# Optimization experiments

Hardware: AMD Instinct MI355X
Metric: run time of the kernel (lower is better)

## Reference

```python
import jax, jax.numpy as jnp
import numpy as np

N, E, IN_DIM, HID, OUT = 50000, 800000, 128, 128, 64


def setup_inputs() -> dict:
    key = jax.random.key(0)
    k = jax.random.split(key, 6)
    h = jax.random.normal(k[0], (N, IN_DIM), dtype=jnp.float32)
    edge_index = jax.random.randint(k[1], (2, E), 0, N, dtype=jnp.int64)
    s_in, s_hid = 1.0 / np.sqrt(IN_DIM), 1.0 / np.sqrt(HID)
    W_gcn = jax.random.uniform(k[2], (IN_DIM, HID), jnp.float32, -s_in, s_in)
    b_gcn = jnp.zeros((HID,), jnp.float32)
    W_fc = jax.random.uniform(k[3], (HID, OUT), jnp.float32, -s_hid, s_hid)
    b_fc = jax.random.uniform(k[4], (OUT,), jnp.float32, -s_hid, s_hid)
    return {"h": h, "edge_index": edge_index, "W_gcn": W_gcn,
            "b_gcn": b_gcn, "W_fc": W_fc, "b_fc": b_fc}


def reference(h, edge_index, W_gcn, b_gcn, W_fc, b_fc):
    n = h.shape[0]
    # GCNConv: transform, add self-loops, symmetric normalization, scatter-add
    x = h @ W_gcn                                   # [N, HID]
    loop = jnp.arange(n, dtype=edge_index.dtype)
    row = jnp.concatenate([edge_index[0], loop])    # source nodes
    col = jnp.concatenate([edge_index[1], loop])    # destination nodes
    deg = jax.ops.segment_sum(jnp.ones_like(col, dtype=x.dtype), col,
                              num_segments=n)       # in-degree incl. self-loop
    dinv = jnp.where(deg > 0, jax.lax.rsqrt(deg), 0.0)
    norm = dinv[row] * dinv[col]                    # [E+N]
    msg = x[row] * norm[:, None]                    # gather + scale
    agg = jax.ops.segment_sum(msg, col, num_segments=n) + b_gcn
    # ReLU then projection
    return jax.nn.relu(agg) @ W_fc + b_fc
```

## Files before the change

kernel.cpp:

```cpp
#include <hip/hip_runtime.h>

#define N_NODES 50000
#define N_EDGES 800000
#define NBKT 782
#define BINB 196
#define CASTB 391
#define SLOTC 20
#define SBKT (BINB * SLOTC)
#define BCAP 1792
#define ESTRIDE 1792
#define SECAP 1792
#define UTS 136

typedef __attribute__((ext_vector_type(4))) float floatx4;
typedef __attribute__((ext_vector_type(8))) _Float16 half8;
typedef __attribute__((ext_vector_type(4))) _Float16 half4;
typedef __attribute__((ext_vector_type(2))) _Float16 half2v;

#define O_C     0UL
#define O_DEG   613120UL
#define O_PTR   813184UL
#define O_W1    1013248UL
#define O_W2    1046016UL
#define O_ESRC  1062400UL
#define O_STG   3865216UL
#define O_H16   16126976UL

__global__ __launch_bounds__(256) void k_bin(const int* __restrict__ ei,
                                             const float* __restrict__ h,
                                             int* __restrict__ C,
                                             unsigned* __restrict__ staging,
                                             const float* __restrict__ Wg,
                                             const float* __restrict__ Wf,
                                             _Float16* __restrict__ W1,
                                             _Float16* __restrict__ W2,
                                             _Float16* __restrict__ h16) {
    int b = blockIdx.x, t = threadIdx.x;
    if (b >= BINB + 96) {
        int wb = b - (BINB + 96);
        int nb = wb * 128;
        int nn = min(128, N_NODES - nb);
        if (nn <= 0) return;
        const floatx4* src = (const floatx4*)(h + (size_t)nb * 128);
        half4* dst = (half4*)(h16 + (size_t)nb * 128);
        int nq = nn * 32;
        for (int i = t; i < nq; i += 256) {
            floatx4 v = src[i];
            half4 o;
            o[0] = (_Float16)v[0]; o[1] = (_Float16)v[1];
            o[2] = (_Float16)v[2]; o[3] = (_Float16)v[3];
            dst[i] = o;
        }
        return;
    }
    if (b >= BINB) {
        int wb = b - BINB;
        if (wb < 64) {
            int i = wb * 256 + t;
            int n = i >> 7, k = i & 127;
            W1[i] = (_Float16)Wg[k * 128 + n];
        } else {
            int i = (wb - 64) * 256 + t;
            int n = i >> 7, k = i & 127;
            W2[i] = (_Float16)Wf[k * 64 + n];
        }
        return;
    }
    __shared__ int cnt[NBKT];
    __shared__ int s_i64;
    if (t < 64) {
        unsigned w = ((const unsigned*)ei)[2 * t + 1];
        unsigned long long m = __ballot(w == 0u);
        if (t == 0) s_i64 = (__popcll(m) >= 60) ? 1 : 0;
    }
    for (int i = t; i < NBKT; i += 256) cnt[i] = 0;
    __syncthreads();
    bool i64 = s_i64 != 0;
    int e0 = b * 4096 + t * 16;
    int sv[16], dvv[16];
    if (i64) {
        const int4* ps = (const int4*)(ei) + (e0 >> 1);
        const int4* pd = (const int4*)(ei + 2 * (size_t)N_EDGES) + (e0 >> 1);
#pragma unroll
        for (int g = 0; g < 8; ++g) {
            if (e0 + 2 * g < N_EDGES) {
                int4 s4 = ps[g], d4 = pd[g];
                sv[2 * g] = s4.x; sv[2 * g + 1] = s4.z;
                dvv[2 * g] = d4.x; dvv[2 * g + 1] = d4.z;
            } else { dvv[2 * g] = -1; dvv[2 * g + 1] = -1; }
        }
    } else {
        const int4* ps = (const int4*)(ei) + (e0 >> 2);
        const int4* pd = (const int4*)(ei + (size_t)N_EDGES) + (e0 >> 2);
#pragma unroll
        for (int g = 0; g < 4; ++g) {
            if (e0 + 4 * g < N_EDGES) {
                int4 s4 = ps[g], d4 = pd[g];
                sv[4 * g] = s4.x; sv[4 * g + 1] = s4.y; sv[4 * g + 2] = s4.z; sv[4 * g + 3] = s4.w;
                dvv[4 * g] = d4.x; dvv[4 * g + 1] = d4.y; dvv[4 * g + 2] = d4.z; dvv[4 * g + 3] = d4.w;
            } else { dvv[4 * g] = -1; dvv[4 * g + 1] = -1; dvv[4 * g + 2] = -1; dvv[4 * g + 3] = -1; }
        }
    }
    unsigned pk[16]; int rk[16]; short bk[16];
#pragma unroll
    for (int j = 0; j < 16; ++j) {
        int d = dvv[j];
        if (d >= 0 && e0 + j < N_EDGES) {
            int bkt = d >> 6;
            bk[j] = (short)bkt;
            pk[j] = (unsigned)sv[j] | ((unsigned)(d & 63) << 16);
            rk[j] = atomicAdd(&cnt[bkt], 1);
        } else bk[j] = -1;
    }
    __syncthreads();
    for (int i = t; i < NBKT; i += 256)
        C[(size_t)b * NBKT + i] = cnt[i];
#pragma unroll
    for (int j = 0; j < 16; ++j) {
        if (bk[j] >= 0 && rk[j] < SLOTC)
            staging[(size_t)bk[j] * SBKT + b * SLOTC + rk[j]] = pk[j];
    }
}

__global__ __launch_bounds__(256) void k_sort(const unsigned* __restrict__ staging,
                                              const int* __restrict__ C,
                                              int* __restrict__ ptr,
                                              int* __restrict__ deg_g,
                                              unsigned short* __restrict__ esrc) {
    __shared__ unsigned se[BCAP];
    __shared__ int lcnt[64];
    __shared__ int cur[64];
    __shared__ int rbase[BINB];
    __shared__ int rcnt[BINB];
    __shared__ int wsum[4];
    __shared__ int s_tot;
    int b = blockIdx.x, t = threadIdx.x;
    int nbase = b * 64;
    int nn = min(64, N_NODES - nbase);
    if (nn <= 0) return;
    int lane = t & 63, wid = t >> 6;
    if (t < 64) lcnt[t] = 0;
    int c = (t < BINB) ? min(C[(size_t)t * NBKT + b], SLOTC) : 0;
    int x = c;
#pragma unroll
    for (int off = 1; off < 64; off <<= 1) {
        int y = __shfl_up(x, off);
        if (lane >= off) x += y;
    }
    if (lane == 63) wsum[wid] = x;
    __syncthreads();
    int wpre = 0;
#pragma unroll
    for (int w = 0; w < 4; ++w) if (w < wid) wpre += wsum[w];
    int excl = wpre + x - c;
    if (t < BINB) { rbase[t] = excl; rcnt[t] = c; }
    if (t == BINB - 1) s_tot = excl + c;
    __syncthreads();
    if (t < BINB && c > 0) {
        const unsigned* sp = staging + (size_t)b * SBKT + t * SLOTC;
        int rb = rbase[t];
        for (int k = 0; k < c; ++k) {
            unsigned p = sp[k];
            if (rb + k < BCAP) {
                se[rb + k] = p;
                atomicAdd(&lcnt[p >> 16], 1);
            }
        }
    }
    __syncthreads();
    if (t < 64) {
        int v = lcnt[t];
        int xx = v;
#pragma unroll
        for (int off = 1; off < 64; off <<= 1) {
            int y = __shfl_up(xx, off);
            if (t >= off) xx += y;
        }
        int seg = xx - v;
        if (t < nn) {
            ptr[nbase + t] = b * ESTRIDE + seg;
            deg_g[nbase + t] = v;
        }
        cur[t] = seg;
    }
    __syncthreads();
    int tot = min(s_tot, BCAP);
    unsigned short* eb = esrc + (size_t)b * ESTRIDE;
    for (int i = t; i < tot; i += 256) {
        unsigned p = se[i];
        int pos = atomicAdd(&cur[p >> 16], 1);
        if (pos < ESTRIDE) eb[pos] = (unsigned short)(p & 0xffffu);
    }
}

__global__ __launch_bounds__(256, 8) void k_aggF(const _Float16* __restrict__ h16,
                                                 const int* __restrict__ ptr,
                                                 const int* __restrict__ deg_g,
                                                 const unsigned short* __restrict__ esrc,
                                                 const _Float16* __restrict__ W1,
                                                 const _Float16* __restrict__ W2,
                                                 const float* __restrict__ bg,
                                                 const float* __restrict__ bfc,
                                                 float* __restrict__ out) {
    __shared__ _Float16 ut[16 * UTS];
    __shared__ _Float16 z[16 * UTS];
    __shared__ unsigned se32[SECAP];
    __shared__ int p16[17];
    __shared__ int deg16[16];
    __shared__ float sdv16[16];
    int t = threadIdx.x;
    int wave = t >> 6;
    int lane = t & 63;
    int nb = blockIdx.x * 16;
    if (t < 16) {
        int dg = deg_g[nb + t];
        deg16[t] = dg;
        sdv16[t] = rsqrtf((float)(dg + 1));
        p16[t] = ptr[nb + t];
    }
    __syncthreads();
    if (t == 0) p16[16] = p16[15] + deg16[15];
    __syncthreads();
    int base0 = p16[0];
    int total = p16[16] - base0;
    if (total > SECAP) total = SECAP;
    for (int i = t; i < total; i += 256) {
        unsigned src = esrc[base0 + i];
        unsigned dg = (unsigned)deg_g[src];
        se32[i] = (dg << 16) | src;
    }
    __syncthreads();
    for (int q = 0; q < 4; ++q) {
        int tag = wave * 4 + q;
        int node = nb + tag;
        int p0 = p16[tag] - base0;
        int p1 = p0 + deg16[tag];
        if (p1 > SECAP) p1 = SECAP;
        float sc = sdv16[tag];
        half2v us = *(const half2v*)(h16 + (size_t)node * 128 + lane * 2);
        float a0 = (float)us[0] * sc, a1 = (float)us[1] * sc;
        for (int base = p0; base < p1; base += 64) {
            int c = p1 - base; if (c > 64) c = 64;
            int idx = 0;
            if (lane < c) idx = (int)se32[base + lane];
            float wf = rsqrtf((float)((unsigned)idx >> 16) + 1.f);
            int j = 0;
            for (; j + 8 <= c; j += 8) {
                int s0 = __shfl(idx, j),     s1 = __shfl(idx, j + 1);
                int s2 = __shfl(idx, j + 2), s3 = __shfl(idx, j + 3);
                int s4 = __shfl(idx, j + 4), s5 = __shfl(idx, j + 5);
                int s6 = __shfl(idx, j + 6), s7 = __shfl(idx, j + 7);
                float f0 = __shfl(wf, j),     f1 = __shfl(wf, j + 1);
                float f2 = __shfl(wf, j + 2), f3 = __shfl(wf, j + 3);
                float f4 = __shfl(wf, j + 4), f5 = __shfl(wf, j + 5);
                float f6 = __shfl(wf, j + 6), f7 = __shfl(wf, j + 7);
                half2v u0 = *(const half2v*)(h16 + (size_t)(s0 & 0xFFFF) * 128 + lane * 2);
                half2v u1 = *(const half2v*)(h16 + (size_t)(s1 & 0xFFFF) * 128 + lane * 2);
                half2v u2 = *(const half2v*)(h16 + (size_t)(s2 & 0xFFFF) * 128 + lane * 2);
                half2v u3 = *(const half2v*)(h16 + (size_t)(s3 & 0xFFFF) * 128 + lane * 2);
                half2v u4 = *(const half2v*)(h16 + (size_t)(s4 & 0xFFFF) * 128 + lane * 2);
                half2v u5 = *(const half2v*)(h16 + (size_t)(s5 & 0xFFFF) * 128 + lane * 2);
                half2v u6 = *(const half2v*)(h16 + (size_t)(s6 & 0xFFFF) * 128 + lane * 2);
                half2v u7 = *(const half2v*)(h16 + (size_t)(s7 & 0xFFFF) * 128 + lane * 2);
                a0 = fmaf((float)u0[0], f0, a0); a1 = fmaf((float)u0[1], f0, a1);
                a0 = fmaf((float)u1[0], f1, a0); a1 = fmaf((float)u1[1], f1, a1);
                a0 = fmaf((float)u2[0], f2, a0); a1 = fmaf((float)u2[1], f2, a1);
                a0 = fmaf((float)u3[0], f3, a0); a1 = fmaf((float)u3[1], f3, a1);
                a0 = fmaf((float)u4[0], f4, a0); a1 = fmaf((float)u4[1], f4, a1);
                a0 = fmaf((float)u5[0], f5, a0); a1 = fmaf((float)u5[1], f5, a1);
                a0 = fmaf((float)u6[0], f6, a0); a1 = fmaf((float)u6[1], f6, a1);
                a0 = fmaf((float)u7[0], f7, a0); a1 = fmaf((float)u7[1], f7, a1);
            }
            for (; j + 4 <= c; j += 4) {
                int s0 = __shfl(idx, j),     s1 = __shfl(idx, j + 1);
                int s2 = __shfl(idx, j + 2), s3 = __shfl(idx, j + 3);
                float f0 = __shfl(wf, j),     f1 = __shfl(wf, j + 1);
                float f2 = __shfl(wf, j + 2), f3 = __shfl(wf, j + 3);
                half2v u0 = *(const half2v*)(h16 + (size_t)(s0 & 0xFFFF) * 128 + lane * 2);
                half2v u1 = *(const half2v*)(h16 + (size_t)(s1 & 0xFFFF) * 128 + lane * 2);
                half2v u2 = *(const half2v*)(h16 + (size_t)(s2 & 0xFFFF) * 128 + lane * 2);
                half2v u3 = *(const half2v*)(h16 + (size_t)(s3 & 0xFFFF) * 128 + lane * 2);
                a0 = fmaf((float)u0[0], f0, a0); a1 = fmaf((float)u0[1], f0, a1);
                a0 = fmaf((float)u1[0], f1, a0); a1 = fmaf((float)u1[1], f1, a1);
                a0 = fmaf((float)u2[0], f2, a0); a1 = fmaf((float)u2[1], f2, a1);
                a0 = fmaf((float)u3[0], f3, a0); a1 = fmaf((float)u3[1], f3, a1);
            }
            for (; j < c; ++j) {
                int s = __shfl(idx, j);
                float f = __shfl(wf, j);
                half2v uu = *(const half2v*)(h16 + (size_t)(s & 0xFFFF) * 128 + lane * 2);
                a0 = fmaf((float)uu[0], f, a0); a1 = fmaf((float)uu[1], f, a1);
            }
        }
        int r = wave * 4 + q;
        ut[r * UTS + lane * 2]     = (_Float16)(a0 * sc);
        ut[r * UTS + lane * 2 + 1] = (_Float16)(a1 * sc);
    }
    __syncthreads();
    int quad = lane >> 4, l15 = lane & 15;
    half8 a[4];
#pragma unroll
    for (int kk = 0; kk < 4; ++kk)
        a[kk] = *(const half8*)(ut + l15 * UTS + kk * 32 + quad * 8);
#pragma unroll
    for (int tt = 0; tt < 2; ++tt) {
        floatx4 acc = {0.f, 0.f, 0.f, 0.f};
        int n = (wave * 2 + tt) * 16 + l15;
#pragma unroll
        for (int kk = 0; kk < 4; ++kk) {
            half8 bb = *(const half8*)(W1 + n * 128 + kk * 32 + quad * 8);
            acc = __builtin_amdgcn_mfma_f32_16x16x32_f16(a[kk], bb, acc, 0, 0, 0);
        }
        float bias = bg[n];
#pragma unroll
        for (int i = 0; i < 4; ++i)
            z[(quad * 4 + i) * UTS + n] = (_Float16)fmaxf(acc[i] + bias, 0.f);
    }
    __syncthreads();
    half8 a2[4];
#pragma unroll
    for (int kk = 0; kk < 4; ++kk)
        a2[kk] = *(const half8*)(z + l15 * UTS + kk * 32 + quad * 8);
    {
        floatx4 acc = {0.f, 0.f, 0.f, 0.f};
        int n = wave * 16 + l15;
#pragma unroll
        for (int kk = 0; kk < 4; ++kk) {
            half8 bb = *(const half8*)(W2 + n * 128 + kk * 32 + quad * 8);
            acc = __builtin_amdgcn_mfma_f32_16x16x32_f16(a2[kk], bb, acc, 0, 0, 0);
        }
        float bias = bfc[n];
#pragma unroll
        for (int i = 0; i < 4; ++i)
            out[(size_t)(nb + quad * 4 + i) * 64 + n] = acc[i] + bias;
    }
}

extern "C" void kernel_launch(void* const* d_in, const int* in_sizes, int n_in,
                              void* d_out, int out_size, void* d_ws, size_t ws_size,
                              hipStream_t stream) {
    (void)in_sizes; (void)n_in; (void)out_size; (void)ws_size;
    const float* h  = (const float*)d_in[0];
    const int*   ei = (const int*)d_in[1];
    const float* Wg = (const float*)d_in[2];
    const float* bg = (const float*)d_in[3];
    const float* Wf = (const float*)d_in[4];
    const float* bf = (const float*)d_in[5];
    float* out = (float*)d_out;

    char* ws = (char*)d_ws;
    int*      C     = (int*)(ws + O_C);
    int*      deg_g = (int*)(ws + O_DEG);
    int*      ptr   = (int*)(ws + O_PTR);
    _Float16* W1    = (_Float16*)(ws + O_W1);
    _Float16* W2    = (_Float16*)(ws + O_W2);
    unsigned short* esrc = (unsigned short*)(ws + O_ESRC);
    unsigned* staging = (unsigned*)(ws + O_STG);
    _Float16* h16   = (_Float16*)(ws + O_H16);

    k_bin<<<BINB + 96 + CASTB, 256, 0, stream>>>(ei, h, C, staging,
                                                 Wg, Wf, W1, W2, h16);
    k_sort<<<NBKT, 256, 0, stream>>>(staging, C, ptr, deg_g, esrc);
    k_aggF<<<N_NODES / 16, 256, 0, stream>>>(h16, ptr, deg_g, esrc,
                                             W1, W2, bg, bf, out);
}
```

Measured before the change: 147.4 us.

## Locally sort edges per bin block into contiguous staging with offset table

The binning kernel now handles 2048 edges per block with twice as many blocks. Each block counting-sorts its edges by destination bucket in shared memory and writes them as one contiguous run, along with a per-bucket exclusive offset table. The sort kernel reads those offsets to find each block's slice, replacing the fixed 20-slot per-bucket staging that was scattered and could drop overflow edges. This gives coalesced staging writes and a smaller staging buffer, at the cost of extra shared-memory prefix sums and more blocks for the sort kernel to read from.

```diff
diff --git a/kernel.cpp b/kernel.cpp
--- a/kernel.cpp
+++ b/kernel.cpp
@@ -3,10 +3,9 @@
 #define N_NODES 50000
 #define N_EDGES 800000
 #define NBKT 782
-#define BINB 196
+#define BINB 392
 #define CASTB 391
-#define SLOTC 20
-#define SBKT (BINB * SLOTC)
+#define OSTRIDE 783
 #define BCAP 1792
 #define ESTRIDE 1792
 #define SECAP 1792
@@ -17,18 +16,18 @@
 typedef __attribute__((ext_vector_type(4))) _Float16 half4;
 typedef __attribute__((ext_vector_type(2))) _Float16 half2v;
 
-#define O_C     0UL
-#define O_DEG   613120UL
-#define O_PTR   813184UL
-#define O_W1    1013248UL
-#define O_W2    1046016UL
-#define O_ESRC  1062400UL
-#define O_STG   3865216UL
-#define O_H16   16126976UL
+#define O_O     0UL
+#define O_DEG   1228288UL
+#define O_PTR   1428480UL
+#define O_W1    1628672UL
+#define O_W2    1661440UL
+#define O_ESRC  1677824UL
+#define O_STG   4480512UL
+#define O_H16   7691776UL
 
 __global__ __launch_bounds__(256) void k_bin(const int* __restrict__ ei,
                                              const float* __restrict__ h,
-                                             int* __restrict__ C,
+                                             int* __restrict__ O,
                                              unsigned* __restrict__ staging,
                                              const float* __restrict__ Wg,
                                              const float* __restrict__ Wf,
@@ -66,23 +65,26 @@
         }
         return;
     }
-    __shared__ int cnt[NBKT];
-    __shared__ int s_i64;
+    __shared__ int cnt[784];
+    __shared__ int base[784];
+    __shared__ unsigned se[2048];
+    __shared__ int wsum[4];
+    __shared__ int s_i64, s_tot;
     if (t < 64) {
         unsigned w = ((const unsigned*)ei)[2 * t + 1];
         unsigned long long m = __ballot(w == 0u);
         if (t == 0) s_i64 = (__popcll(m) >= 60) ? 1 : 0;
     }
-    for (int i = t; i < NBKT; i += 256) cnt[i] = 0;
+    for (int i = t; i < 784; i += 256) cnt[i] = 0;
     __syncthreads();
     bool i64 = s_i64 != 0;
-    int e0 = b * 4096 + t * 16;
-    int sv[16], dvv[16];
+    int e0 = b * 2048 + t * 8;
+    int sv[8], dvv[8];
     if (i64) {
         const int4* ps = (const int4*)(ei) + (e0 >> 1);
         const int4* pd = (const int4*)(ei + 2 * (size_t)N_EDGES) + (e0 >> 1);
 #pragma unroll
-        for (int g = 0; g < 8; ++g) {
+        for (int g = 0; g < 4; ++g) {
             if (e0 + 2 * g < N_EDGES) {
                 int4 s4 = ps[g], d4 = pd[g];
                 sv[2 * g] = s4.x; sv[2 * g + 1] = s4.z;
@@ -93,7 +95,7 @@
         const int4* ps = (const int4*)(ei) + (e0 >> 2);
         const int4* pd = (const int4*)(ei + (size_t)N_EDGES) + (e0 >> 2);
 #pragma unroll
-        for (int g = 0; g < 4; ++g) {
+        for (int g = 0; g < 2; ++g) {
             if (e0 + 4 * g < N_EDGES) {
                 int4 s4 = ps[g], d4 = pd[g];
                 sv[4 * g] = s4.x; sv[4 * g + 1] = s4.y; sv[4 * g + 2] = s4.z; sv[4 * g + 3] = s4.w;
@@ -101,9 +103,9 @@
             } else { dvv[4 * g] = -1; dvv[4 * g + 1] = -1; dvv[4 * g + 2] = -1; dvv[4 * g + 3] = -1; }
         }
     }
-    unsigned pk[16]; int rk[16]; short bk[16];
-#pragma unroll
-    for (int j = 0; j < 16; ++j) {
+    unsigned pk[8]; int rk[8]; short bk[8];
+#pragma unroll
+    for (int j = 0; j < 8; ++j) {
         int d = dvv[j];
         if (d >= 0 && e0 + j < N_EDGES) {
             int bkt = d >> 6;
@@ -113,25 +115,54 @@
         } else bk[j] = -1;
     }
     __syncthreads();
-    for (int i = t; i < NBKT; i += 256)
-        C[(size_t)b * NBKT + i] = cnt[i];
-#pragma unroll
-    for (int j = 0; j < 16; ++j) {
-        if (bk[j] >= 0 && rk[j] < SLOTC)
-            staging[(size_t)bk[j] * SBKT + b * SLOTC + rk[j]] = pk[j];
-    }
+    int c0 = 0, c1 = 0, c2 = 0, c3 = 0, s = 0;
+    if (t < 196) {
+        int tb = t * 4;
+        c0 = cnt[tb]; c1 = cnt[tb + 1]; c2 = cnt[tb + 2]; c3 = cnt[tb + 3];
+        s = c0 + c1 + c2 + c3;
+    }
+    int lane = t & 63, wid = t >> 6;
+    int x = s;
+#pragma unroll
+    for (int off = 1; off < 64; off <<= 1) {
+        int y = __shfl_up(x, off);
+        if (lane >= off) x += y;
+    }
+    if (lane == 63) wsum[wid] = x;
+    __syncthreads();
+    int wpre = 0;
+#pragma unroll
+    for (int w = 0; w < 4; ++w) if (w < wid) wpre += wsum[w];
+    int excl = wpre + x - s;
+    if (t < 196) {
+        int tb = t * 4;
+        base[tb]     = excl;
+        base[tb + 1] = excl + c0;
+        base[tb + 2] = excl + c0 + c1;
+        base[tb + 3] = excl + c0 + c1 + c2;
+    }
+    if (t == 255) s_tot = excl + s;
+    __syncthreads();
+#pragma unroll
+    for (int j = 0; j < 8; ++j)
+        if (bk[j] >= 0) se[base[bk[j]] + rk[j]] = pk[j];
+    __syncthreads();
+    int tot = s_tot;
+    for (int i = t; i < tot; i += 256)
+        staging[(size_t)b * 2048 + i] = se[i];
+    for (int i = t; i < OSTRIDE; i += 256)
+        O[(size_t)b * OSTRIDE + i] = base[i];
 }
 
 __global__ __launch_bounds__(256) void k_sort(const unsigned* __restrict__ staging,
-                                              const int* __restrict__ C,
+                                              const int* __restrict__ O,
                                               int* __restrict__ ptr,
                                               int* __restrict__ deg_g,
                                               unsigned short* __restrict__ esrc) {
     __shared__ unsigned se[BCAP];
     __shared__ int lcnt[64];
     __shared__ int cur[64];
-    __shared__ int rbase[BINB];
-    __shared__ int rcnt[BINB];
+    __shared__ int rb[BINB], rc[BINB], rof[BINB];
     __shared__ int wsum[4];
     __shared__ int s_tot;
     int b = blockIdx.x, t = threadIdx.x;
@@ -140,8 +171,18 @@
     if (nn <= 0) return;
     int lane = t & 63, wid = t >> 6;
     if (t < 64) lcnt[t] = 0;
-    int c = (t < BINB) ? min(C[(size_t)t * NBKT + b], SLOTC) : 0;
-    int x = c;
+    int blk0 = 2 * t, blk1 = 2 * t + 1;
+    int c0 = 0, c1 = 0, o0 = 0, o1 = 0;
+    if (blk0 < BINB) {
+        const int* Or = O + (size_t)blk0 * OSTRIDE;
+        o0 = Or[b]; c0 = Or[b + 1] - o0;
+    }
+    if (blk1 < BINB) {
+        const int* Or = O + (size_t)blk1 * OSTRIDE;
+        o1 = Or[b]; c1 = Or[b + 1] - o1;
+    }
+    int s = c0 + c1;
+    int x = s;
 #pragma unroll
     for (int off = 1; off < 64; off <<= 1) {
         int y = __shfl_up(x, off);
@@ -152,17 +193,19 @@
     int wpre = 0;
 #pragma unroll
     for (int w = 0; w < 4; ++w) if (w < wid) wpre += wsum[w];
-    int excl = wpre + x - c;
-    if (t < BINB) { rbase[t] = excl; rcnt[t] = c; }
-    if (t == BINB - 1) s_tot = excl + c;
-    __syncthreads();
-    if (t < BINB && c > 0) {
-        const unsigned* sp = staging + (size_t)b * SBKT + t * SLOTC;
-        int rb = rbase[t];
+    int excl = wpre + x - s;
+    if (blk0 < BINB) { rb[blk0] = excl;      rc[blk0] = c0; rof[blk0] = o0; }
+    if (blk1 < BINB) { rb[blk1] = excl + c0; rc[blk1] = c1; rof[blk1] = o1; }
+    if (t == 255) s_tot = excl + s;
+    __syncthreads();
+    for (int blk = t; blk < BINB; blk += 256) {
+        int c = rc[blk]; int rbs = rb[blk];
+        const unsigned* sp = staging + (size_t)blk * 2048 + rof[blk];
         for (int k = 0; k < c; ++k) {
-            unsigned p = sp[k];
-            if (rb + k < BCAP) {
-                se[rb + k] = p;
+            int pos = rbs + k;
+            if (pos < BCAP) {
+                unsigned p = sp[k];
+                se[pos] = p;
                 atomicAdd(&lcnt[p >> 16], 1);
             }
         }
@@ -349,7 +392,7 @@
     float* out = (float*)d_out;
 
     char* ws = (char*)d_ws;
-    int*      C     = (int*)(ws + O_C);
+    int*      O     = (int*)(ws + O_O);
     int*      deg_g = (int*)(ws + O_DEG);
     int*      ptr   = (int*)(ws + O_PTR);
     _Float16* W1    = (_Float16*)(ws + O_W1);
@@ -358,9 +401,9 @@
     unsigned* staging = (unsigned*)(ws + O_STG);
     _Float16* h16   = (_Float16*)(ws + O_H16);
 
-    k_bin<<<BINB + 96 + CASTB, 256, 0, stream>>>(ei, h, C, staging,
+    k_bin<<<BINB + 96 + CASTB, 256, 0, stream>>>(ei, h, O, staging,
                                                  Wg, Wf, W1, W2, h16);
-    k_sort<<<NBKT, 256, 0, stream>>>(staging, C, ptr, deg_g, esrc);
+    k_sort<<<NBKT, 256, 0, stream>>>(staging, O, ptr, deg_g, esrc);
     k_aggF<<<N_NODES / 16, 256, 0, stream>>>(h16, ptr, deg_g, esrc,
                                              W1, W2, bg, bf, out);
 }
```

Measured after the change: 151.0 us. 1.02x slower.
